# Optimization experiments

Measured on AMD Instinct MI355X. Metric: run time of the kernel, lower is better.

Reference implementation:

```python
import jax, jax.numpy as jnp
import numpy as np

# dims
B, QL, KL = 2, 1024, 4096
HID = 2048            # hidden_size
H, HD, RD = 16, 128, 64   # heads, head_dim, rope_dim
G = 4                 # gla_num_groups
HPG = H // G          # heads_per_group
QLR = 512             # q low-rank (W_dQ out)
LAT = 256             # latent_dim_per_group
KVP = G * LAT         # kv_proj_dim
EPS = 1e-6


def rmsnorm(x, w):
    var = jnp.mean(jnp.square(x.astype(jnp.float32)), axis=-1, keepdims=True)
    return (x * jax.lax.rsqrt(var + EPS)).astype(x.dtype) * w


def setup_inputs() -> dict:
    key = jax.random.key(0)
    ks = jax.random.split(key, 8)
    s = 0.02
    return {
        "x_q": jax.random.normal(ks[0], (B, QL, HID), jnp.float32),
        "x_kv": jax.random.normal(ks[1], (B, KL, HID), jnp.float32),
        "W_dQ": jax.random.normal(ks[2], (HID, QLR), jnp.float32) * s,
        "q_norm_w": jnp.ones((QLR,), jnp.float32),
        "W_uQ": jax.random.normal(ks[3], (QLR, H * (HD + RD)), jnp.float32) * s,
        "W_dKV": jax.random.normal(ks[4], (HID, KVP + RD), jnp.float32) * s,
        "kv_norm_w": jnp.ones((G, LAT), jnp.float32),
        "W_ukv": jax.random.normal(ks[5], (G, LAT, HPG * 2 * HD), jnp.float32) * s,
        "W_o": jax.random.normal(ks[6], (H * HD, HID), jnp.float32) * s,
    }


def reference(x_q, x_kv, W_dQ, q_norm_w, W_uQ, W_dKV, kv_norm_w, W_ukv, W_o):
    b, ql, _ = x_q.shape
    kl = x_kv.shape[1]
    # --- query path: down-proj -> RMSNorm -> up-proj -> drop rope dims ---
    q = rmsnorm(x_q @ W_dQ, q_norm_w)                       # [b, ql, QLR]
    q = (q @ W_uQ).reshape(b, ql, H, HD + RD)[..., :HD]     # [b, ql, H, HD]
    # --- kv path: down-proj -> slice -> per-group RMSNorm -> grouped up-proj ---
    ckv = (x_kv @ W_dKV)[..., :KVP].reshape(b, kl, G, LAT)  # [b, kl, G, LAT]
    ckv = rmsnorm(ckv, kv_norm_w)                           # weight [G, LAT] broadcasts
    kv = jnp.einsum("bsgl,gld->bsgd", ckv, W_ukv)           # [b, kl, G, HPG*2*HD]
    kv = kv.reshape(b, kl, H, 2 * HD)                       # group-major head order
    k, v = kv[..., :HD], kv[..., HD:]
    # --- SDPA (no mask, non-causal) ---
    scale = 1.0 / np.sqrt(HD).astype(np.float32)
    scores = jnp.einsum("bqhd,bkhd->bhqk", q, k) * scale    # [b, H, ql, kl]
    p = jax.nn.softmax(scores, axis=-1)
    out = jnp.einsum("bhqk,bkhd->bqhd", p, v).reshape(b, ql, H * HD)
    return out @ W_o
```

## Files before the change

kernel.cpp:

```cpp
#include <hip/hip_runtime.h>
#include <hip/hip_bf16.h>
#include <math.h>


typedef __attribute__((ext_vector_type(8))) short short8;
typedef __attribute__((ext_vector_type(4))) float f32x4;

__device__ __forceinline__ ushort f2bf(float x) {
    __hip_bfloat16 h = __float2bfloat16(x);
    return *reinterpret_cast<ushort*>(&h);
}

#define SWZ(row, col) ((col) ^ (((row) & 7) << 3))

__device__ __forceinline__ void gload16(const ushort* g, ushort* l)
{
    __builtin_amdgcn_global_load_lds(
        (const __attribute__((address_space(1))) void*)g,
        (__attribute__((address_space(3))) void*)l, 16, 0, 0);
}

__global__ __launch_bounds__(256) void cast_bf16(const float* __restrict__ src,
        ushort* __restrict__ dst)
{
    size_t i = ((size_t)blockIdx.x * 256 + threadIdx.x) * 8;
    float4 a = *(const float4*)(src + i);
    float4 b = *(const float4*)(src + i + 4);
    ushort u[8] = {f2bf(a.x), f2bf(a.y), f2bf(a.z), f2bf(a.w),
                   f2bf(b.x), f2bf(b.y), f2bf(b.z), f2bf(b.w)};
    *(uint4*)(dst + i) = *(uint4*)u;
}

__global__ __launch_bounds__(256) void transpose_cast(const float* __restrict__ src,
        ushort* __restrict__ dst, int srl, int dstld, int remap,
        long src_z, long dst_z)
{
    __shared__ ushort tile[64][68];
    const int k0 = blockIdx.x * 64;
    const int n0 = blockIdx.y * 64;
    src += (size_t)blockIdx.z * src_z;
    dst += (size_t)blockIdx.z * dst_z;
    const int cb = n0 + (remap ? (n0 >> 7) * 64 : 0);
    const int t = threadIdx.x;
    {
        int r = t >> 4, c4 = t & 15;
        #pragma unroll
        for (int i = 0; i < 4; ++i) {
            float4 v = *(const float4*)(src + (size_t)(k0 + r + 16 * i) * srl + cb + c4 * 4);
            tile[r + 16 * i][c4 * 4 + 0] = f2bf(v.x);
            tile[r + 16 * i][c4 * 4 + 1] = f2bf(v.y);
            tile[r + 16 * i][c4 * 4 + 2] = f2bf(v.z);
            tile[r + 16 * i][c4 * 4 + 3] = f2bf(v.w);
        }
    }
    __syncthreads();
    {
        int n = t >> 4, k4 = t & 15;
        #pragma unroll
        for (int i = 0; i < 4; ++i) {
            ushort4 v;
            v.x = tile[k4 * 4 + 0][n + 16 * i];
            v.y = tile[k4 * 4 + 1][n + 16 * i];
            v.z = tile[k4 * 4 + 2][n + 16 * i];
            v.w = tile[k4 * 4 + 3][n + 16 * i];
            *(ushort4*)(dst + (size_t)(n0 + n + 16 * i) * dstld + k0 + k4 * 4) = v;
        }
    }
}

__global__ __launch_bounds__(256) void gemm_mfma(const ushort* __restrict__ A,
        const ushort* __restrict__ Bt, void* __restrict__ Cv,
        int M, int N, int K, int lda, int ldb, int ldc, int obf16, float scale)
{
    __shared__ ushort As[128 * 64];
    __shared__ ushort Bs[128 * 64];
    const int tid = threadIdx.x;
    const int w = tid >> 6, lane = tid & 63;
    const int quad = lane >> 4, l16 = lane & 15;
    const int wm = (w >> 1) * 64, wn = (w & 1) * 64;
    const int m0 = blockIdx.y * 128, n0 = blockIdx.x * 128;

    f32x4 acc[4][4];
    #pragma unroll
    for (int i = 0; i < 4; ++i)
        #pragma unroll
        for (int j = 0; j < 4; ++j) acc[i][j] = (f32x4){0.f, 0.f, 0.f, 0.f};

    const int srow = lane >> 3;
    const int scol = ((lane & 7) * 8) ^ ((srow & 7) << 3);

    for (int k0 = 0; k0 < K; k0 += 64) {
        __syncthreads();
        #pragma unroll
        for (int i = 0; i < 4; ++i) {
            int r = w * 32 + i * 8 + srow;
            gload16(A + (size_t)(m0 + r) * lda + k0 + scol, &As[w * 2048 + i * 512]);
            gload16(Bt + (size_t)(n0 + r) * ldb + k0 + scol, &Bs[w * 2048 + i * 512]);
        }
        __syncthreads();
        #pragma unroll
        for (int kc = 0; kc < 2; ++kc) {
            short8 af[4], bf[4];
            #pragma unroll
            for (int i = 0; i < 4; ++i) {
                int ra = wm + i * 16 + l16;
                int rb = wn + i * 16 + l16;
                af[i] = *(const short8*)&As[ra * 64 + SWZ(ra, kc * 32 + quad * 8)];
                bf[i] = *(const short8*)&Bs[rb * 64 + SWZ(rb, kc * 32 + quad * 8)];
            }
            #pragma unroll
            for (int i = 0; i < 4; ++i)
                #pragma unroll
                for (int j = 0; j < 4; ++j)
                    acc[i][j] = __builtin_amdgcn_mfma_f32_16x16x32_bf16(af[i], bf[j], acc[i][j], 0, 0, 0);
        }
    }
    if (!obf16) {
        float* C = (float*)Cv;
        #pragma unroll
        for (int i = 0; i < 4; ++i)
            #pragma unroll
            for (int r = 0; r < 4; ++r) {
                float* cp = C + (size_t)(m0 + wm + i * 16 + quad * 4 + r) * ldc + n0 + wn + l16;
                #pragma unroll
                for (int j = 0; j < 4; ++j) cp[j * 16] = acc[i][j][r] * scale;
            }
    } else {
        ushort* C = (ushort*)Cv;
        #pragma unroll
        for (int i = 0; i < 4; ++i)
            #pragma unroll
            for (int r = 0; r < 4; ++r) {
                ushort* cp = C + (size_t)(m0 + wm + i * 16 + quad * 4 + r) * ldc + n0 + wn + l16;
                #pragma unroll
                for (int j = 0; j < 4; ++j) cp[j * 16] = f2bf(acc[i][j][r] * scale);
            }
    }
}

__global__ __launch_bounds__(256) void rms_q_wave(const float* __restrict__ x,
        const float* __restrict__ w, ushort* __restrict__ dst)
{
    const int row = blockIdx.x * 4 + (threadIdx.x >> 6);
    const int lane = threadIdx.x & 63;
    const float* p = x + (size_t)row * 512;
    float4 v0 = *(const float4*)(p + lane * 4);
    float4 v1 = *(const float4*)(p + 256 + lane * 4);
    float ss = v0.x*v0.x + v0.y*v0.y + v0.z*v0.z + v0.w*v0.w
             + v1.x*v1.x + v1.y*v1.y + v1.z*v1.z + v1.w*v1.w;
    #pragma unroll
    for (int m = 1; m < 64; m <<= 1) ss += __shfl_xor(ss, m);
    float inv = rsqrtf(ss * (1.f / 512.f) + 1e-6f);
    float4 w0 = *(const float4*)(w + lane * 4);
    float4 w1 = *(const float4*)(w + 256 + lane * 4);
    ushort* dp = dst + (size_t)row * 512;
    ushort4 o0, o1;
    o0.x = f2bf(v0.x * inv * w0.x); o0.y = f2bf(v0.y * inv * w0.y);
    o0.z = f2bf(v0.z * inv * w0.z); o0.w = f2bf(v0.w * inv * w0.w);
    o1.x = f2bf(v1.x * inv * w1.x); o1.y = f2bf(v1.y * inv * w1.y);
    o1.z = f2bf(v1.z * inv * w1.z); o1.w = f2bf(v1.w * inv * w1.w);
    *(ushort4*)(dp + lane * 4)       = o0;
    *(ushort4*)(dp + 256 + lane * 4) = o1;
}

__global__ __launch_bounds__(256) void rms_kv_wave(const float* __restrict__ x,
        const float* __restrict__ w, ushort* __restrict__ dst)
{
    const int idx = blockIdx.x * 4 + (threadIdx.x >> 6);
    const int lane = threadIdx.x & 63;
    const int r = idx >> 2, g = idx & 3;
    const float* p = x + (size_t)r * 1024 + g * 256;
    float4 v = *(const float4*)(p + lane * 4);
    float ss = v.x*v.x + v.y*v.y + v.z*v.z + v.w*v.w;
    #pragma unroll
    for (int m = 1; m < 64; m <<= 1) ss += __shfl_xor(ss, m);
    float inv = rsqrtf(ss * (1.f / 256.f) + 1e-6f);
    float4 wv = *(const float4*)(w + g * 256 + lane * 4);
    ushort4 o;
    o.x = f2bf(v.x * inv * wv.x); o.y = f2bf(v.y * inv * wv.y);
    o.z = f2bf(v.z * inv * wv.z); o.w = f2bf(v.w * inv * wv.w);
    *(ushort4*)(dst + (size_t)r * 1024 + g * 256 + lane * 4) = o;
}

__global__ __launch_bounds__(256) void transpose_v(const ushort* __restrict__ KVb,
                                                   ushort* __restrict__ Vt)
{
    __shared__ ushort tile[64][66];
    const int s0 = blockIdx.x * 64;
    const int d0 = blockIdx.y * 64;
    const int bh = blockIdx.z;
    const int b = bh >> 4, h = bh & 15, g = h >> 2, p = h & 3;
    const int t = threadIdx.x;
    const ushort* src = KVb + (size_t)g * 8388608ull + (size_t)(b * 4096) * 1024 + p * 256 + 128;
    {
        int sl = t >> 4, c4 = t & 15;
        #pragma unroll
        for (int i = 0; i < 4; ++i) {
            int s = sl + 16 * i;
            ushort4 v = *(const ushort4*)(src + (size_t)(s0 + s) * 1024 + d0 + c4 * 4);
            tile[s][c4 * 4 + 0] = v.x; tile[s][c4 * 4 + 1] = v.y;
            tile[s][c4 * 4 + 2] = v.z; tile[s][c4 * 4 + 3] = v.w;
        }
    }
    __syncthreads();
    {
        int dl = t >> 4, s4 = t & 15;
        ushort* dst = Vt + (size_t)(b * 16 + h) * 128 * 4096;
        #pragma unroll
        for (int i = 0; i < 4; ++i) {
            int d = dl + 16 * i;
            ushort4 v;
            v.x = tile[s4 * 4 + 0][d]; v.y = tile[s4 * 4 + 1][d];
            v.z = tile[s4 * 4 + 2][d]; v.w = tile[s4 * 4 + 3][d];
            *(ushort4*)(dst + (size_t)(d0 + d) * 4096 + s0 + s4 * 4) = v;
        }
    }
}

#define ATTN_STAGE(KS, VS, S0) do {                                            \
    _Pragma("unroll")                                                          \
    for (int i_ = 0; i_ < 4; ++i_) {                                           \
        int r_ = w * 16 + i_ * 4 + k_r4;                                       \
        gload16(kg + (size_t)((S0) + r_) * 1024 + (k_cb ^ ((r_ & 7) << 3)),    \
                &KS[w * 2048 + i_ * 512]);                                     \
    }                                                                          \
    _Pragma("unroll")                                                          \
    for (int i_ = 0; i_ < 4; ++i_) {                                           \
        int d_ = w * 32 + i_ * 8 + v_r8;                                       \
        gload16(vg + (size_t)d_ * 4096 + (S0) + v_c,                           \
                &VS[w * 2048 + i_ * 512]);                                     \
    }                                                                          \
} while (0)

#define ATTN_COMPUTE(KS, VS) do {                                              \
    f32x4 accS[4];                                                             \
    _Pragma("unroll")                                                          \
    for (int st = 0; st < 4; ++st) accS[st] = (f32x4){0.f, 0.f, 0.f, 0.f};     \
    __builtin_amdgcn_s_setprio(1);                                             \
    _Pragma("unroll")                                                          \
    for (int kc = 0; kc < 4; ++kc) {                                           \
        _Pragma("unroll")                                                      \
        for (int st = 0; st < 4; ++st) {                                       \
            int krow = st * 16 + l16;                                          \
            short8 kf = *(const short8*)&KS[krow * 128 + SWZ(krow, kc * 32 + quad * 8)]; \
            accS[st] = __builtin_amdgcn_mfma_f32_16x16x32_bf16(qf[kc], kf, accS[st], 0, 0, 0); \
        }                                                                      \
    }                                                                          \
    __builtin_amdgcn_s_setprio(0);                                             \
    _Pragma("unroll")                                                          \
    for (int r = 0; r < 4; ++r) {                                              \
        float tm = fmaxf(fmaxf(accS[0][r], accS[1][r]), fmaxf(accS[2][r], accS[3][r])); \
        _Pragma("unroll")                                                      \
        for (int msk = 1; msk < 16; msk <<= 1) tm = fmaxf(tm, __shfl_xor(tm, msk)); \
        if (tm > m_i[r] + 8.f) {                                               \
            float alpha = __expf(m_i[r] - tm);                                 \
            l_i[r] *= alpha;                                                   \
            _Pragma("unroll")                                                  \
            for (int dt = 0; dt < 8; ++dt) accO[dt][r] *= alpha;               \
            m_i[r] = tm;                                                       \
        }                                                                      \
        const float mn = m_i[r];                                               \
        float rs = 0.f;                                                        \
        const int prow = quad * 4 + r;                                         \
        _Pragma("unroll")                                                      \
        for (int st = 0; st < 4; ++st) {                                       \
            float e = __expf(accS[st][r] - mn);                                \
            rs += e;                                                           \
            Ps[(w * 16 + prow) * 64 + SWZ(prow, st * 16 + l16)] = f2bf(e);     \
        }                                                                      \
        _Pragma("unroll")                                                      \
        for (int msk = 1; msk < 16; msk <<= 1) rs += __shfl_xor(rs, msk);      \
        l_i[r] += rs;                                                          \
    }                                                                          \
    short8 pf[2];                                                              \
    _Pragma("unroll")                                                          \
    for (int sc = 0; sc < 2; ++sc)                                             \
        pf[sc] = *(const short8*)&Ps[(w * 16 + l16) * 64 + SWZ(l16, sc * 32 + quad * 8)]; \
    __builtin_amdgcn_s_setprio(1);                                             \
    _Pragma("unroll")                                                          \
    for (int sc = 0; sc < 2; ++sc) {                                           \
        _Pragma("unroll")                                                      \
        for (int dt = 0; dt < 8; ++dt) {                                       \
            int vrow = dt * 16 + l16;                                          \
            short8 vf = *(const short8*)&VS[vrow * 64 + SWZ(vrow, sc * 32 + quad * 8)]; \
            accO[dt] = __builtin_amdgcn_mfma_f32_16x16x32_bf16(pf[sc], vf, accO[dt], 0, 0, 0); \
        }                                                                      \
    }                                                                          \
    __builtin_amdgcn_s_setprio(0);                                             \
} while (0)

__global__ __launch_bounds__(256) void attn_mfma_split(const ushort* __restrict__ Qb,
        const ushort* __restrict__ KVb, const ushort* __restrict__ Vt,
        float* __restrict__ Opart, float* __restrict__ ml)
{
    __shared__ ushort Ks0[64 * 128];
    __shared__ ushort Ks1[64 * 128];
    __shared__ ushort Vs0[128 * 64];
    __shared__ ushort Vs1[128 * 64];
    __shared__ ushort Ps[4 * 16 * 64];

    const int q0 = blockIdx.x * 64;
    const int h = blockIdx.y;
    const int b = blockIdx.z >> 1, chunk = blockIdx.z & 1;
    const int g = h >> 2, p = h & 3;
    const int tid = threadIdx.x;
    const int w = tid >> 6, lane = tid & 63;
    const int quad = lane >> 4, l16 = lane & 15;
    const int sbase = chunk * 2048;

    const ushort* qg = Qb + (size_t)(b * 1024 + q0) * 2048 + h * 128;
    const ushort* kg = KVb + (size_t)g * 8388608ull + (size_t)(b * 4096 + sbase) * 1024 + p * 256;
    const ushort* vg = Vt + (size_t)(b * 16 + h) * 128 * 4096 + sbase;

    const int k_r4 = lane >> 4;
    const int k_cb = (lane & 15) * 8;
    const int v_r8 = lane >> 3;
    const int v_c  = ((lane & 7) * 8) ^ ((v_r8 & 7) << 3);

    {
        int kr = tid >> 4, kc8 = (tid & 15) * 8;
        #pragma unroll
        for (int i = 0; i < 4; ++i) {
            int r = kr + 16 * i;
            *(uint4*)&Ks0[r * 128 + SWZ(r, kc8)] = *(const uint4*)(qg + (size_t)r * 2048 + kc8);
        }
    }
    __syncthreads();
    short8 qf[4];
    {
        int qr = w * 16 + l16;
        #pragma unroll
        for (int kc = 0; kc < 4; ++kc)
            qf[kc] = *(const short8*)&Ks0[qr * 128 + SWZ(qr, kc * 32 + quad * 8)];
    }
    ATTN_STAGE(Ks1, Vs1, 0);
    __syncthreads();

    f32x4 accO[8];
    float m_i[4], l_i[4];
    #pragma unroll
    for (int dt = 0; dt < 8; ++dt) accO[dt] = (f32x4){0.f, 0.f, 0.f, 0.f};
    #pragma unroll
    for (int r = 0; r < 4; ++r) { m_i[r] = -INFINITY; l_i[r] = 0.f; }

    for (int it = 0; it < 16; ++it) {
        const int s0 = it * 128;
        ATTN_STAGE(Ks0, Vs0, s0 + 64);
        ATTN_COMPUTE(Ks1, Vs1);
        __syncthreads();
        if (it < 15) ATTN_STAGE(Ks1, Vs1, s0 + 128);
        ATTN_COMPUTE(Ks0, Vs0);
        __syncthreads();
    }

    const int qrow = q0 + w * 16 + quad * 4;
    float* ob = Opart + (size_t)((chunk * 2 + b) * 1024 + qrow) * 2048 + h * 128 + l16;
    #pragma unroll
    for (int r = 0; r < 4; ++r)
        #pragma unroll
        for (int dt = 0; dt < 8; ++dt)
            ob[(size_t)r * 2048 + dt * 16] = accO[dt][r];
    if (l16 == 0) {
        #pragma unroll
        for (int r = 0; r < 4; ++r) {
            size_t mi = ((size_t)((chunk * 2 + b) * 1024 + qrow + r) * 16 + h) * 2;
            ml[mi] = m_i[r];
            ml[mi + 1] = l_i[r];
        }
    }
}

__global__ __launch_bounds__(256) void attn_merge(const float* __restrict__ Opart,
        const float* __restrict__ ml, ushort* __restrict__ Om)
{
    const int idx = blockIdx.x * 4 + (threadIdx.x >> 6);
    const int lane = threadIdx.x & 63;
    const int h = idx & 15;
    const int q = (idx >> 4) & 1023;
    const int b = idx >> 14;

    size_t m1i = ((size_t)((0 * 2 + b) * 1024 + q) * 16 + h) * 2;
    size_t m2i = ((size_t)((1 * 2 + b) * 1024 + q) * 16 + h) * 2;
    float m1 = ml[m1i], l1 = ml[m1i + 1];
    float m2 = ml[m2i], l2 = ml[m2i + 1];
    float M = fmaxf(m1, m2);
    float w1 = __expf(m1 - M), w2 = __expf(m2 - M);
    float invL = 1.f / (l1 * w1 + l2 * w2);

    const float* o1 = Opart + (size_t)((0 * 2 + b) * 1024 + q) * 2048 + h * 128;
    const float* o2 = Opart + (size_t)((1 * 2 + b) * 1024 + q) * 2048 + h * 128;
    ushort* ob = Om + (size_t)(b * 1024 + q) * 2048 + h * 128;
    ob[lane]      = f2bf((o1[lane]      * w1 + o2[lane]      * w2) * invL);
    ob[lane + 64] = f2bf((o1[lane + 64] * w1 + o2[lane + 64] * w2) * invL);
}

extern "C" void kernel_launch(void* const* d_in, const int* in_sizes, int n_in,
                              void* d_out, int out_size, void* d_ws, size_t ws_size,
                              hipStream_t stream)
{
    (void)in_sizes; (void)n_in; (void)out_size; (void)ws_size;
    const float* x_q       = (const float*)d_in[0];
    const float* x_kv      = (const float*)d_in[1];
    const float* W_dQ      = (const float*)d_in[2];
    const float* q_norm_w  = (const float*)d_in[3];
    const float* W_uQ      = (const float*)d_in[4];
    const float* W_dKV     = (const float*)d_in[5];
    const float* kv_norm_w = (const float*)d_in[6];
    const float* W_ukv     = (const float*)d_in[7];
    const float* W_o       = (const float*)d_in[8];
    float* out = (float*)d_out;

    float* ws = (float*)d_ws;
    ushort* xkvb       = (ushort*)ws;
    ushort* attn_out_b = (ushort*)ws;
    float*  mlbuf      = ws + 2097152ull;
    ushort* Wot        = (ushort*)(ws + 4194304ull);
    float*  ckv        = ws + 8388608ull;
    float*  Opart      = ws + 8388608ull;
    ushort* xqb        = (ushort*)(ws + 8388608ull);
    ushort* WdQt       = (ushort*)(ws + 10485760ull);
    float*  q_lat      = ws + 11010048ull;
    ushort* q_lat_b    = (ushort*)(ws + 12058624ull);
    ushort* WuQt       = (ushort*)(ws + 12582912ull);
    ushort* ckv_b      = (ushort*)(ws + 16777216ull);
    ushort* kvgb       = (ushort*)(ws + 20971520ull);
    ushort* vt         = (ushort*)(ws + 37748736ull);
    ushort* qb         = (ushort*)(ws + 46137344ull);
    ushort* WdKVt      = (ushort*)(ws + 48234496ull);
    ushort* Wukvt      = (ushort*)(ws + 49283072ull);

    const float qscale = 0.08838834764831845f;

    cast_bf16<<<2048, 256, 0, stream>>>(x_q, xqb);
    transpose_cast<<<dim3(32, 8, 1), 256, 0, stream>>>(W_dQ, WdQt, 512, 2048, 0, 0, 0);
    gemm_mfma<<<dim3(4, 16), 256, 0, stream>>>(xqb, WdQt, q_lat, 2048, 512, 2048, 2048, 2048, 512, 0, 1.f);
    rms_q_wave<<<512, 256, 0, stream>>>(q_lat, q_norm_w, q_lat_b);
    transpose_cast<<<dim3(8, 32, 1), 256, 0, stream>>>(W_uQ, WuQt, 3072, 512, 1, 0, 0);
    gemm_mfma<<<dim3(16, 16), 256, 0, stream>>>(q_lat_b, WuQt, qb, 2048, 2048, 512, 512, 512, 2048, 1, qscale);
    cast_bf16<<<8192, 256, 0, stream>>>(x_kv, xkvb);
    transpose_cast<<<dim3(32, 16, 1), 256, 0, stream>>>(W_dKV, WdKVt, 1088, 2048, 0, 0, 0);
    gemm_mfma<<<dim3(8, 64), 256, 0, stream>>>(xkvb, WdKVt, ckv, 8192, 1024, 2048, 2048, 2048, 1024, 0, 1.f);
    rms_kv_wave<<<8192, 256, 0, stream>>>(ckv, kv_norm_w, ckv_b);
    transpose_cast<<<dim3(4, 16, 4), 256, 0, stream>>>(W_ukv, Wukvt, 1024, 256, 0, 262144, 262144);
    for (int g = 0; g < 4; ++g)
        gemm_mfma<<<dim3(8, 64), 256, 0, stream>>>(ckv_b + g * 256, Wukvt + (size_t)g * 262144,
                                                   kvgb + (size_t)g * 8388608ull,
                                                   8192, 1024, 256, 1024, 256, 1024, 1, 1.f);
    transpose_v<<<dim3(64, 2, 32), 256, 0, stream>>>(kvgb, vt);
    attn_mfma_split<<<dim3(16, 16, 4), 256, 0, stream>>>(qb, kvgb, vt, Opart, mlbuf);
    attn_merge<<<8192, 256, 0, stream>>>(Opart, mlbuf, attn_out_b);
    transpose_cast<<<dim3(32, 32, 1), 256, 0, stream>>>(W_o, Wot, 2048, 2048, 0, 0, 0);
    gemm_mfma<<<dim3(16, 16), 256, 0, stream>>>(attn_out_b, Wot, out, 2048, 2048, 2048, 2048, 2048, 2048, 0, 1.f);
}
```

Baseline: 559.4 us.

## Replace LDS double-buffered async loads with register-staged prefetch in attention

The attention kernel drops its two LDS buffers filled by direct global-to-LDS async loads. It now prefetches the next K/V tile into registers during compute and writes it into a single LDS buffer each iteration. This halves LDS use, which may allow more resident blocks. In exchange it adds register pressure and two barriers per 64-key tile instead of one.

After: 722.6 us. +29.2%, slower.

```diff
diff --git a/kernel.cpp b/kernel.cpp
--- a/kernel.cpp
+++ b/kernel.cpp
@@ -217,22 +217,7 @@
     }
 }
 
-#define ATTN_STAGE(KS, VS, S0) do {                                            \
-    _Pragma("unroll")                                                          \
-    for (int i_ = 0; i_ < 4; ++i_) {                                           \
-        int r_ = w * 16 + i_ * 4 + k_r4;                                       \
-        gload16(kg + (size_t)((S0) + r_) * 1024 + (k_cb ^ ((r_ & 7) << 3)),    \
-                &KS[w * 2048 + i_ * 512]);                                     \
-    }                                                                          \
-    _Pragma("unroll")                                                          \
-    for (int i_ = 0; i_ < 4; ++i_) {                                           \
-        int d_ = w * 32 + i_ * 8 + v_r8;                                       \
-        gload16(vg + (size_t)d_ * 4096 + (S0) + v_c,                           \
-                &VS[w * 2048 + i_ * 512]);                                     \
-    }                                                                          \
-} while (0)
-
-#define ATTN_COMPUTE(KS, VS) do {                                              \
+#define ATTN_COMPUTE() do {                                                    \
     f32x4 accS[4];                                                             \
     _Pragma("unroll")                                                          \
     for (int st = 0; st < 4; ++st) accS[st] = (f32x4){0.f, 0.f, 0.f, 0.f};     \
@@ -242,7 +227,7 @@
         _Pragma("unroll")                                                      \
         for (int st = 0; st < 4; ++st) {                                       \
             int krow = st * 16 + l16;                                          \
-            short8 kf = *(const short8*)&KS[krow * 128 + SWZ(krow, kc * 32 + quad * 8)]; \
+            short8 kf = *(const short8*)&Ks[krow * 128 + SWZ(krow, kc * 32 + quad * 8)]; \
             accS[st] = __builtin_amdgcn_mfma_f32_16x16x32_bf16(qf[kc], kf, accS[st], 0, 0, 0); \
         }                                                                      \
     }                                                                          \
@@ -282,7 +267,7 @@
         _Pragma("unroll")                                                      \
         for (int dt = 0; dt < 8; ++dt) {                                       \
             int vrow = dt * 16 + l16;                                          \
-            short8 vf = *(const short8*)&VS[vrow * 64 + SWZ(vrow, sc * 32 + quad * 8)]; \
+            short8 vf = *(const short8*)&VsT[vrow * 64 + SWZ(vrow, sc * 32 + quad * 8)]; \
             accO[dt] = __builtin_amdgcn_mfma_f32_16x16x32_bf16(pf[sc], vf, accO[dt], 0, 0, 0); \
         }                                                                      \
     }                                                                          \
@@ -293,10 +278,8 @@
         const ushort* __restrict__ KVb, const ushort* __restrict__ Vt,
         float* __restrict__ Opart, float* __restrict__ ml)
 {
-    __shared__ ushort Ks0[64 * 128];
-    __shared__ ushort Ks1[64 * 128];
-    __shared__ ushort Vs0[128 * 64];
-    __shared__ ushort Vs1[128 * 64];
+    __shared__ ushort Ks[64 * 128];
+    __shared__ ushort VsT[128 * 64];
     __shared__ ushort Ps[4 * 16 * 64];
 
     const int q0 = blockIdx.x * 64;
@@ -312,18 +295,23 @@
     const ushort* kg = KVb + (size_t)g * 8388608ull + (size_t)(b * 4096 + sbase) * 1024 + p * 256;
     const ushort* vg = Vt + (size_t)(b * 16 + h) * 128 * 4096 + sbase;
 
-    const int k_r4 = lane >> 4;
-    const int k_cb = (lane & 15) * 8;
-    const int v_r8 = lane >> 3;
-    const int v_c  = ((lane & 7) * 8) ^ ((v_r8 & 7) << 3);
-
-    {
-        int kr = tid >> 4, kc8 = (tid & 15) * 8;
-        #pragma unroll
-        for (int i = 0; i < 4; ++i) {
-            int r = kr + 16 * i;
-            *(uint4*)&Ks0[r * 128 + SWZ(r, kc8)] = *(const uint4*)(qg + (size_t)r * 2048 + kc8);
-        }
+    const int kr  = tid >> 4;
+    const int kc8 = (tid & 15) * 8;
+    const int vd  = tid >> 3;
+    const int vs8 = (tid & 7) * 8;
+
+    uint4 krg[4], vrg[4];
+    #pragma unroll
+    for (int i = 0; i < 4; ++i)
+        krg[i] = *(const uint4*)(kg + (size_t)(kr + 16 * i) * 1024 + kc8);
+    #pragma unroll
+    for (int i = 0; i < 4; ++i)
+        vrg[i] = *(const uint4*)(vg + (size_t)(vd + 32 * i) * 4096 + vs8);
+
+    #pragma unroll
+    for (int i = 0; i < 4; ++i) {
+        int r = kr + 16 * i;
+        *(uint4*)&Ks[r * 128 + SWZ(r, kc8)] = *(const uint4*)(qg + (size_t)r * 2048 + kc8);
     }
     __syncthreads();
     short8 qf[4];
@@ -331,10 +319,8 @@
         int qr = w * 16 + l16;
         #pragma unroll
         for (int kc = 0; kc < 4; ++kc)
-            qf[kc] = *(const short8*)&Ks0[qr * 128 + SWZ(qr, kc * 32 + quad * 8)];
-    }
-    ATTN_STAGE(Ks1, Vs1, 0);
-    __syncthreads();
+            qf[kc] = *(const short8*)&Ks[qr * 128 + SWZ(qr, kc * 32 + quad * 8)];
+    }
 
     f32x4 accO[8];
     float m_i[4], l_i[4];
@@ -343,14 +329,28 @@
     #pragma unroll
     for (int r = 0; r < 4; ++r) { m_i[r] = -INFINITY; l_i[r] = 0.f; }
 
-    for (int it = 0; it < 16; ++it) {
-        const int s0 = it * 128;
-        ATTN_STAGE(Ks0, Vs0, s0 + 64);
-        ATTN_COMPUTE(Ks1, Vs1);
+    for (int s0 = 0; s0 < 2048; s0 += 64) {
         __syncthreads();
-        if (it < 15) ATTN_STAGE(Ks1, Vs1, s0 + 128);
-        ATTN_COMPUTE(Ks0, Vs0);
+        #pragma unroll
+        for (int i = 0; i < 4; ++i) {
+            int r = kr + 16 * i;
+            *(uint4*)&Ks[r * 128 + SWZ(r, kc8)] = krg[i];
+        }
+        #pragma unroll
+        for (int i = 0; i < 4; ++i) {
+            int d = vd + 32 * i;
+            *(uint4*)&VsT[d * 64 + SWZ(d, vs8)] = vrg[i];
+        }
         __syncthreads();
+        if (s0 + 64 < 2048) {
+            #pragma unroll
+            for (int i = 0; i < 4; ++i)
+                krg[i] = *(const uint4*)(kg + (size_t)(s0 + 64 + kr + 16 * i) * 1024 + kc8);
+            #pragma unroll
+            for (int i = 0; i < 4; ++i)
+                vrg[i] = *(const uint4*)(vg + (size_t)(vd + 32 * i) * 4096 + s0 + 64 + vs8);
+        }
+        ATTN_COMPUTE();
     }
 
     const int qrow = q0 + w * 16 + quad * 4;
```

## Pipeline attention K/V loads with vmcnt waits and batch grouped up-proj GEMMs

Applied to the files above, without the earlier changes.

The attention kernel's K/V double buffering is restructured. Both buffers are prefetched up front, and each __syncthreads is replaced by raw s_barrier plus explicit s_waitcnt vmcnt(8), so the next tile's async loads stay in flight while the current tile is computed. The four per-group KV up-projection GEMM launches are merged into one launch using blockIdx.z with per-z pointer strides, which cuts launch overhead and fills the grid better. The partial vmcnt counts depend on how many loads ATTN_STAGE issues, so a wrong count would cause data races.

New measurement: 556.9 us. Within noise of the previous version (-0.5%).

```diff
diff --git a/kernel.cpp b/kernel.cpp
--- a/kernel.cpp
+++ b/kernel.cpp
@@ -70,10 +70,14 @@
 
 __global__ __launch_bounds__(256) void gemm_mfma(const ushort* __restrict__ A,
         const ushort* __restrict__ Bt, void* __restrict__ Cv,
-        int M, int N, int K, int lda, int ldb, int ldc, int obf16, float scale)
+        int M, int N, int K, int lda, int ldb, int ldc, int obf16, float scale,
+        long a_z, long b_z, long c_z)
 {
     __shared__ ushort As[128 * 64];
     __shared__ ushort Bs[128 * 64];
+    A  += (size_t)blockIdx.z * a_z;
+    Bt += (size_t)blockIdx.z * b_z;
+    Cv  = (void*)((char*)Cv + (size_t)blockIdx.z * c_z);
     const int tid = threadIdx.x;
     const int w = tid >> 6, lane = tid & 63;
     const int quad = lane >> 4, l16 = lane & 15;
@@ -289,13 +293,18 @@
     __builtin_amdgcn_s_setprio(0);                                             \
 } while (0)
 
+#define WAITVM(N) do {                                                         \
+    asm volatile("s_waitcnt vmcnt(" #N ")" ::: "memory");                      \
+    __builtin_amdgcn_sched_barrier(0);                                         \
+} while (0)
+
 __global__ __launch_bounds__(256) void attn_mfma_split(const ushort* __restrict__ Qb,
         const ushort* __restrict__ KVb, const ushort* __restrict__ Vt,
         float* __restrict__ Opart, float* __restrict__ ml)
 {
     __shared__ ushort Ks0[64 * 128];
+    __shared__ ushort Vs0[128 * 64];
     __shared__ ushort Ks1[64 * 128];
-    __shared__ ushort Vs0[128 * 64];
     __shared__ ushort Vs1[128 * 64];
     __shared__ ushort Ps[4 * 16 * 64];
 
@@ -333,7 +342,6 @@
         for (int kc = 0; kc < 4; ++kc)
             qf[kc] = *(const short8*)&Ks0[qr * 128 + SWZ(qr, kc * 32 + quad * 8)];
     }
-    ATTN_STAGE(Ks1, Vs1, 0);
     __syncthreads();
 
     f32x4 accO[8];
@@ -343,15 +351,28 @@
     #pragma unroll
     for (int r = 0; r < 4; ++r) { m_i[r] = -INFINITY; l_i[r] = 0.f; }
 
-    for (int it = 0; it < 16; ++it) {
-        const int s0 = it * 128;
-        ATTN_STAGE(Ks0, Vs0, s0 + 64);
+    ATTN_STAGE(Ks0, Vs0, 0);
+    ATTN_STAGE(Ks1, Vs1, 64);
+    WAITVM(8);
+    __builtin_amdgcn_s_barrier();
+
+    for (int it2 = 0; it2 < 15; ++it2) {
+        const int t0 = it2 * 2;
+        ATTN_COMPUTE(Ks0, Vs0);
+        __builtin_amdgcn_s_barrier();
+        ATTN_STAGE(Ks0, Vs0, (t0 + 2) * 64);
+        WAITVM(8);
+        __builtin_amdgcn_s_barrier();
         ATTN_COMPUTE(Ks1, Vs1);
-        __syncthreads();
-        if (it < 15) ATTN_STAGE(Ks1, Vs1, s0 + 128);
-        ATTN_COMPUTE(Ks0, Vs0);
-        __syncthreads();
-    }
+        __builtin_amdgcn_s_barrier();
+        ATTN_STAGE(Ks1, Vs1, (t0 + 3) * 64);
+        WAITVM(8);
+        __builtin_amdgcn_s_barrier();
+    }
+    ATTN_COMPUTE(Ks0, Vs0);
+    WAITVM(0);
+    __builtin_amdgcn_s_barrier();
+    ATTN_COMPUTE(Ks1, Vs1);
 
     const int qrow = q0 + w * 16 + quad * 4;
     float* ob = Opart + (size_t)((chunk * 2 + b) * 1024 + qrow) * 2048 + h * 128 + l16;
@@ -433,22 +454,21 @@
 
     cast_bf16<<<2048, 256, 0, stream>>>(x_q, xqb);
     transpose_cast<<<dim3(32, 8, 1), 256, 0, stream>>>(W_dQ, WdQt, 512, 2048, 0, 0, 0);
-    gemm_mfma<<<dim3(4, 16), 256, 0, stream>>>(xqb, WdQt, q_lat, 2048, 512, 2048, 2048, 2048, 512, 0, 1.f);
+    gemm_mfma<<<dim3(4, 16), 256, 0, stream>>>(xqb, WdQt, q_lat, 2048, 512, 2048, 2048, 2048, 512, 0, 1.f, 0, 0, 0);
     rms_q_wave<<<512, 256, 0, stream>>>(q_lat, q_norm_w, q_lat_b);
     transpose_cast<<<dim3(8, 32, 1), 256, 0, stream>>>(W_uQ, WuQt, 3072, 512, 1, 0, 0);
-    gemm_mfma<<<dim3(16, 16), 256, 0, stream>>>(q_lat_b, WuQt, qb, 2048, 2048, 512, 512, 512, 2048, 1, qscale);
+    gemm_mfma<<<dim3(16, 16), 256, 0, stream>>>(q_lat_b, WuQt, qb, 2048, 2048, 512, 512, 512, 2048, 1, qscale, 0, 0, 0);
     cast_bf16<<<8192, 256, 0, stream>>>(x_kv, xkvb);
     transpose_cast<<<dim3(32, 16, 1), 256, 0, stream>>>(W_dKV, WdKVt, 1088, 2048, 0, 0, 0);
-    gemm_mfma<<<dim3(8, 64), 256, 0, stream>>>(xkvb, WdKVt, ckv, 8192, 1024, 2048, 2048, 2048, 1024, 0, 1.f);
+    gemm_mfma<<<dim3(8, 64), 256, 0, stream>>>(xkvb, WdKVt, ckv, 8192, 1024, 2048, 2048, 2048, 1024, 0, 1.f, 0, 0, 0);
     rms_kv_wave<<<8192, 256, 0, stream>>>(ckv, kv_norm_w, ckv_b);
     transpose_cast<<<dim3(4, 16, 4), 256, 0, stream>>>(W_ukv, Wukvt, 1024, 256, 0, 262144, 262144);
-    for (int g = 0; g < 4; ++g)
-        gemm_mfma<<<dim3(8, 64), 256, 0, stream>>>(ckv_b + g * 256, Wukvt + (size_t)g * 262144,
-                                                   kvgb + (size_t)g * 8388608ull,
-                                                   8192, 1024, 256, 1024, 256, 1024, 1, 1.f);
+    gemm_mfma<<<dim3(8, 64, 4), 256, 0, stream>>>(ckv_b, Wukvt, kvgb,
+                                                  8192, 1024, 256, 1024, 256, 1024, 1, 1.f,
+                                                  256, 262144, 16777216);
     transpose_v<<<dim3(64, 2, 32), 256, 0, stream>>>(kvgb, vt);
     attn_mfma_split<<<dim3(16, 16, 4), 256, 0, stream>>>(qb, kvgb, vt, Opart, mlbuf);
     attn_merge<<<8192, 256, 0, stream>>>(Opart, mlbuf, attn_out_b);
     transpose_cast<<<dim3(32, 32, 1), 256, 0, stream>>>(W_o, Wot, 2048, 2048, 0, 0, 0);
-    gemm_mfma<<<dim3(16, 16), 256, 0, stream>>>(attn_out_b, Wot, out, 2048, 2048, 2048, 2048, 2048, 2048, 0, 1.f);
-}
+    gemm_mfma<<<dim3(16, 16), 256, 0, stream>>>(attn_out_b, Wot, out, 2048, 2048, 2048, 2048, 2048, 2048, 0, 1.f, 0, 0, 0);
+}
```
